# Kernel optimization log

Measured on AMD Instinct MI355X. Metric: run time of the kernel, lower is better.

Reference implementation:

```python
import jax, jax.numpy as jnp
import numpy as np

B_, N_, D_ = 8, 1024, 64
H_, DH_ = 4, 16
DI_, DS_, DTR_ = 128, 64, 4
MAXP = 512


def _ln(x, w, b, eps=1e-5):
    m = jnp.mean(x, -1, keepdims=True)
    v = jnp.mean((x - m) ** 2, -1, keepdims=True)
    return (x - m) * jax.lax.rsqrt(v + eps) * w + b


def _attn(x, drop_mask, Wq, Wkv, Wo, bo, rel_emb):
    b, n, d = x.shape
    scale = DH_ ** -0.5
    q = (x @ Wq).reshape(b, n, H_, DH_).transpose(0, 2, 1, 3)
    kv = x @ Wkv
    k = kv[..., :d].reshape(b, n, H_, DH_).transpose(0, 2, 1, 3)
    v = kv[..., d:].reshape(b, n, H_, DH_).transpose(0, 2, 1, 3)
    dots = jnp.einsum('bhid,bhjd->bhij', q, k) * scale
    seq = jnp.arange(n)
    dist = jnp.clip(seq[:, None] - seq[None, :], -MAXP, MAXP) + MAXP
    rpe = rel_emb[dist]  # (n, n, DH_)
    dots = dots + jnp.einsum('bhid,ijd->bhij', q, rpe) * scale
    # stochastic key drop: Bernoulli(0.3) positions get -1e12
    dots = dots + drop_mask.astype(dots.dtype) * (-1e12)
    attn = jax.nn.softmax(dots, axis=-1)
    out = jnp.einsum('bhij,bhjd->bhid', attn, v)
    out = out.transpose(0, 2, 1, 3).reshape(b, n, H_ * DH_)
    return out @ Wo + bo


def _mamba(x, W_in, conv_w, conv_b, W_xproj, W_dt, b_dt, A_log, Dm, W_out):
    b, n, _ = x.shape
    xz = x @ W_in                      # (b, n, 2*DI_)
    u, z = xz[..., :DI_], xz[..., DI_:]
    uc = u.transpose(0, 2, 1)          # (b, DI_, n)
    uc = jax.lax.conv_general_dilated(
        uc, conv_w[:, None, :], (1,), ((3, 0),),
        feature_group_count=DI_, dimension_numbers=('NCH', 'OIH', 'NCH'))
    uc = uc + conv_b[None, :, None]
    u = jax.nn.silu(uc).transpose(0, 2, 1)  # (b, n, DI_)
    xdb = u @ W_xproj                  # (b, n, DTR_+2*DS_)
    dt = jax.nn.softplus(xdb[..., :DTR_] @ W_dt + b_dt)  # (b, n, DI_)
    Bm = xdb[..., DTR_:DTR_ + DS_]
    Cm = xdb[..., DTR_ + DS_:]
    A = -jnp.exp(A_log)                # (DI_, DS_)

    def step(h, inp):
        dt_t, B_t, C_t, u_t = inp      # (b,DI_),(b,DS_),(b,DS_),(b,DI_)
        dA = jnp.exp(dt_t[..., None] * A)
        h = h * dA + (dt_t * u_t)[..., None] * B_t[:, None, :]
        y = jnp.einsum('bds,bs->bd', h, C_t)
        return h, y

    h0 = jnp.zeros((b, DI_, DS_), x.dtype)
    xs = (dt.transpose(1, 0, 2), Bm.transpose(1, 0, 2),
          Cm.transpose(1, 0, 2), u.transpose(1, 0, 2))
    _, ys = jax.lax.scan(step, h0, xs)
    y = ys.transpose(1, 0, 2) + u * Dm
    y = y * jax.nn.silu(z)
    return y @ W_out


def _rmsgn(x, gamma, eps=1e-5, groups=4):
    shp = x.shape
    dpg = shp[-1] // groups
    xg = x.reshape(shp[:-1] + (groups, dpg))
    rms = jnp.sqrt(jnp.sum(xg * xg, -1, keepdims=True)) * (dpg ** -0.5)
    return (xg / (rms + eps)).reshape(shp) * gamma


def _ff1(x, c1_w, c1_b, d1_w, d1_b):
    # SwiGLUConvDeconv1d(64, 256, kernel=4, shift=1); x: (b, s2, 64)
    s2 = x.shape[1]
    xc = x.transpose(0, 2, 1)
    xc = jnp.pad(xc, ((0, 0), (0, 0), (3, 3)))
    xc = jax.lax.conv_general_dilated(
        xc, c1_w, (1,), 'VALID', dimension_numbers=('NCH', 'OIH', 'NCH'))
    xc = xc + c1_b[None, :, None]
    gate = jax.nn.silu(xc[:, 256:, :])
    xc = xc[:, :256, :] * gate
    # ConvTranspose1d stride 1 == conv with flipped kernel, full padding
    w = jnp.flip(d1_w, -1).transpose(1, 0, 2)  # (64, 256, 4)
    xc = jax.lax.conv_general_dilated(
        xc, w, (1,), ((3, 3),), dimension_numbers=('NCH', 'OIH', 'NCH'))
    xc = xc + d1_b[None, :, None]
    out = xc.transpose(0, 2, 1)
    return out[:, 3:3 + s2, :]


def _forward(x, drop_mask, ln1_w, ln1_b, Wq, Wkv, Wo, bo, rel_emb,
             ln2_w, ln2_b, W_in, conv_w, conv_b, W_xproj, W_dt, b_dt,
             A_log, Dm, W_out, gamma, c1_w, c1_b, d1_w, d1_b, ln3_w, ln3_b):
    xt = _ln(x, ln1_w, ln1_b)
    xt = _attn(xt, drop_mask, Wq, Wkv, Wo, bo, rel_emb) + x
    x = x + xt  # dropout p=0 -> identity (faithful to original residual math)
    xt = _ln(x, ln2_w, ln2_b)
    m = _mamba(xt, W_in, conv_w, conv_b, W_xproj, W_dt, b_dt, A_log, Dm, W_out)
    m = jnp.where(m >= 0, m, 0.01 * m)  # leaky_relu
    m = _rmsgn(m, gamma)
    m = m + 0.5 * _ff1(m, c1_w, c1_b, d1_w, d1_b)
    x = x + m
    return _ln(x, ln3_w, ln3_b)


def setup_inputs() -> dict:
    ks = jax.random.split(jax.random.key(0), 16)
    g = lambda i, shp, s: jax.random.normal(ks[i], shp, dtype=jnp.float32) * s
    A_log = jnp.log(jnp.tile(jnp.arange(1, DS_ + 1, dtype=jnp.float32)[None, :], (DI_, 1)))
    return {
        'x': jax.random.normal(ks[0], (B_, N_, D_), dtype=jnp.float32),
        'drop_mask': jax.random.bernoulli(ks[1], 0.3, (B_, H_, N_, N_)),
        'ln1_w': jnp.ones((D_,), jnp.float32), 'ln1_b': jnp.zeros((D_,), jnp.float32),
        'Wq': g(2, (D_, D_), 0.1), 'Wkv': g(3, (D_, 2 * D_), 0.1),
        'Wo': g(4, (D_, D_), 0.1), 'bo': jnp.zeros((D_,), jnp.float32),
        'rel_emb': g(5, (2 * MAXP + 1, DH_), 0.02),
        'ln2_w': jnp.ones((D_,), jnp.float32), 'ln2_b': jnp.zeros((D_,), jnp.float32),
        'W_in': g(6, (D_, 2 * DI_), 0.1),
        'conv_w': g(7, (DI_, 4), 0.2), 'conv_b': jnp.zeros((DI_,), jnp.float32),
        'W_xproj': g(8, (DI_, DTR_ + 2 * DS_), 0.1),
        'W_dt': g(9, (DTR_, DI_), 0.1), 'b_dt': jnp.zeros((DI_,), jnp.float32),
        'A_log': A_log, 'Dm': jnp.ones((DI_,), jnp.float32),
        'W_out': g(10, (DI_, D_), 0.1),
        'gamma': jnp.ones((D_,), jnp.float32),
        'c1_w': g(11, (512, 64, 4), 0.1), 'c1_b': jnp.zeros((512,), jnp.float32),
        'd1_w': g(12, (256, 64, 4), 0.1), 'd1_b': jnp.zeros((64,), jnp.float32),
        'ln3_w': jnp.ones((D_,), jnp.float32), 'ln3_b': jnp.zeros((D_,), jnp.float32),
    }


def reference(x, drop_mask, ln1_w, ln1_b, Wq, Wkv, Wo, bo, rel_emb,
              ln2_w, ln2_b, W_in, conv_w, conv_b, W_xproj, W_dt, b_dt,
              A_log, Dm, W_out, gamma, c1_w, c1_b, d1_w, d1_b, ln3_w, ln3_b):
    return _forward(x, drop_mask, ln1_w, ln1_b, Wq, Wkv, Wo, bo, rel_emb,
                    ln2_w, ln2_b, W_in, conv_w, conv_b, W_xproj, W_dt, b_dt,
                    A_log, Dm, W_out, gamma, c1_w, c1_b, d1_w, d1_b, ln3_w, ln3_b)
```

## Files before the change

### kernel.cpp

```cpp
#include <hip/hip_runtime.h>
#include <math.h>


__device__ __forceinline__ float wsum64(float v){
#pragma unroll
  for(int m=32;m>0;m>>=1) v += __shfl_xor(v, m, 64);
  return v;
}
__device__ __forceinline__ float wmax64(float v){
#pragma unroll
  for(int m=32;m>0;m>>=1) v = fmaxf(v, __shfl_xor(v, m, 64));
  return v;
}
__device__ __forceinline__ float silu_f(float x){ return x / (1.f + __expf(-x)); }

__global__ __launch_bounds__(256) void k_ln1_qkv(
    const float* __restrict__ x, const float* __restrict__ w1, const float* __restrict__ b1,
    const float* __restrict__ Wq, const float* __restrict__ Wkv,
    const float* __restrict__ rel, const float* __restrict__ c1w,
    float* __restrict__ qb, float2* __restrict__ kvT,
    float* __restrict__ relT, float* __restrict__ c1wT){
  int lane = threadIdx.x & 63, warp = threadIdx.x >> 6;
  int token = blockIdx.x*4 + warp;
  __shared__ float xt[4][64];
  float xv = x[(size_t)token*64 + lane];
  float mean = wsum64(xv) * 0.015625f;
  float dlt = xv - mean;
  float var = wsum64(dlt*dlt) * 0.015625f;
  float xn = dlt * rsqrtf(var + 1e-5f) * w1[lane] + b1[lane];
  xt[warp][lane] = xn;
  __syncthreads();
  float aq=0.f, ak=0.f, av=0.f;
#pragma unroll 4
  for(int dd=0; dd<64; ++dd){
    float xd = xt[warp][dd];
    aq += xd * Wq[dd*64 + lane];
    ak += xd * Wkv[dd*128 + lane];
    av += xd * Wkv[dd*128 + 64 + lane];
  }
  int b = token >> 10, i = token & 1023;
  int h = lane >> 4, dh = lane & 15;
  size_t o  = (((size_t)(b*4 + h))*1024 + i)*16 + dh;
  size_t oT = (((size_t)(b*4 + h))*16 + dh)*1024 + i;
  qb[o]=aq;
  kvT[oT] = make_float2(ak, av);

  if (blockIdx.x < 65){
    int idx = blockIdx.x*256 + threadIdx.x;
    if (idx < 16*1025){
      int c = idx / 1025;
      int d = idx - c*1025;
      relT[idx] = rel[d*16 + c];
    }
  } else if (blockIdx.x < 577){
    int idx = (blockIdx.x-65)*256 + threadIdx.x;
    int row = idx >> 9;
    int ii  = idx & 511;
    c1wT[idx] = c1w[(size_t)ii*256 + row];
  }
}

__global__ __launch_bounds__(256) void k_kmax_pack(
    const float2* __restrict__ kvT, float* __restrict__ Kmax,
    const int* __restrict__ dmask, unsigned long long* __restrict__ mask64){
  int tid = threadIdx.x;
  if (blockIdx.x >= 32){
    size_t base = (size_t)(blockIdx.x - 32) * 16384;
    const int* dp = dmask + base;
    unsigned long long* mp = mask64 + (base >> 6);
#pragma unroll 4
    for(int r=0;r<64;++r){
      int m = dp[r*256 + tid];
      unsigned long long bal = __ballot(m != 0);
      if ((tid & 63) == 0) mp[r*4 + (tid >> 6)] = bal;
    }
    return;
  }
  int bh = blockIdx.x;
  const float2* base = kvT + (size_t)bh*16*1024;
  float mx = 0.f;
#pragma unroll
  for(int r=0;r<4;++r){
    int j = tid + 256*r;
    float ss = 0.f;
#pragma unroll
    for(int c=0;c<16;++c){ float2 kv = base[c*1024 + j]; ss += kv.x*kv.x; }
    mx = fmaxf(mx, ss);
  }
  mx = wmax64(mx);
  __shared__ float red[4];
  int lane = tid&63, wv = tid>>6;
  if(lane==0) red[wv]=mx;
  __syncthreads();
  if(tid==0) Kmax[bh] = sqrtf(fmaxf(fmaxf(red[0],red[1]),fmaxf(red[2],red[3])));
}

__global__ __launch_bounds__(256, 3) void k_attn(
    const float* __restrict__ qb, const float2* __restrict__ kvT,
    const unsigned long long* __restrict__ mask64, const float* __restrict__ relT,
    const float* __restrict__ Kmax, float* __restrict__ attn_raw){
  int tid = threadIdx.x;
  int lane = tid & 63, wv = tid >> 6;
  int wg   = blockIdx.x;
  int xcd  = wg & 7;
  int slot = wg >> 3;
  int bh   = xcd*4 + (slot >> 7);
  int i0   = (slot & 127) * 8;
  int b = bh >> 2, h = bh & 3;
  int r0 = wv*2, r1 = wv*2 + 1;

  __shared__ float Gc[8][1024];
  __shared__ float qs[8][16];
  __shared__ float G0s[8], G1024s[8];
  __shared__ float gmS[8];
  __shared__ float Ms[8];
  __shared__ float sums[8];

  if (tid < 128){
    int r = tid >> 4, c = tid & 15;
    qs[r][c] = qb[((size_t)bh*1024 + i0 + r)*16 + c] * 0.25f;
  }
  __syncthreads();

#pragma unroll 1
  for(int bb=0; bb<5; ++bb){
    int d = tid + 256*bb;
    if (d <= 1024){
      float rl[16];
#pragma unroll
      for(int c=0;c<16;++c) rl[c] = relT[c*1025 + d];
#pragma unroll
      for(int r=0;r<8;++r){
        float g = 0.f;
#pragma unroll
        for(int c=0;c<16;++c) g += qs[r][c]*rl[c];
        if (d == 0)        G0s[r] = g;
        else if (d == 1024) G1024s[r] = g;
        else {
          int j = i0 + r + 512 - d;
          if (j >= 0 && j < 1024) Gc[r][j] = g;
        }
      }
    }
  }
  __syncthreads();
  {
    const unsigned long long* mrow = mask64 + ((size_t)bh*1024 + i0)*16;
#pragma unroll
    for(int r=0;r<8;++r){
      float g0 = G0s[r], g1 = G1024s[r];
      int lo = i0 + r - 512;
      int hi = i0 + r + 512;
#pragma unroll
      for(int p=0;p<4;++p){
        int j = tid + 256*p;
        unsigned long long w = mrow[r*16 + (j>>6)];
        float g;
        if (j >= hi) g = g0;
        else if (j <= lo) g = g1;
        else g = Gc[r][j];
        if ((w >> (j & 63)) & 1ULL) g = -1e30f;
        Gc[r][j] = g;
      }
    }
  }
  __syncthreads();
  {
    int r = tid >> 5, jb = tid & 31;
    float gm = -3.0e38f;
#pragma unroll
    for(int k=0;k<32;++k) gm = fmaxf(gm, Gc[r][jb + 32*k]);
#pragma unroll
    for(int m=1;m<32;m<<=1) gm = fmaxf(gm, __shfl_xor(gm, m, 64));
    if ((lane&31)==0) gmS[r] = gm;
  }
  __syncthreads();
  if (tid < 8){
    float qn = 0.f;
#pragma unroll
    for(int c=0;c<16;++c) qn += qs[tid][c]*qs[tid][c];
    Ms[tid] = gmS[tid] + sqrtf(qn)*Kmax[bh];
  }
  __syncthreads();

  float q0[16], q1[16];
#pragma unroll
  for(int c=0;c<16;++c){ q0[c]=qs[r0][c]; q1[c]=qs[r1][c]; }
  float M0 = Ms[r0], M1 = Ms[r1];

  const float2* kvb = kvT + (size_t)bh*16*1024;

  float s0=0.f, s1=0.f;
  float a0[16], a1[16];
#pragma unroll
  for(int c=0;c<16;++c){ a0[c]=0.f; a1[c]=0.f; }

#pragma unroll 1
  for(int t=0;t<16;++t){
    int j = lane + 64*t;
    float2 kv[16];
#pragma unroll
    for(int c=0;c<16;++c) kv[c] = kvb[c*1024 + j];
    float sv0 = Gc[r0][j], sv1 = Gc[r1][j];
#pragma unroll
    for(int c=0;c<16;++c){ sv0 += q0[c]*kv[c].x; sv1 += q1[c]*kv[c].x; }
    float p0 = __expf(sv0 - M0);
    float p1 = __expf(sv1 - M1);
    s0 += p0; s1 += p1;
#pragma unroll
    for(int c=0;c<16;++c){ a0[c] += p0*kv[c].y; a1[c] += p1*kv[c].y; }
  }
  s0 = wsum64(s0); s1 = wsum64(s1);
#pragma unroll
  for(int c=0;c<16;++c){
    float x0 = a0[c];
    x0 += __shfl_xor(x0, 32, 64); x0 += __shfl_xor(x0, 16, 64);
    a0[c] = x0;
    float x1 = a1[c];
    x1 += __shfl_xor(x1, 32, 64); x1 += __shfl_xor(x1, 16, 64);
    a1[c] = x1;
  }
  __syncthreads();
  float* red = &Gc[0][0];
  if (lane < 16){
#pragma unroll
    for(int c=0;c<16;++c){
      red[r0*272 + lane*17 + c] = a0[c];
      red[r1*272 + lane*17 + c] = a1[c];
    }
  }
  if (lane == 0){ sums[r0] = s0; sums[r1] = s1; }
  __syncthreads();
  if (tid < 128){
    int row = tid >> 4, c = tid & 15;
    float tot = 0.f;
#pragma unroll
    for(int g=0; g<16; ++g) tot += red[row*272 + g*17 + c];
    attn_raw[((size_t)b*1024 + i0 + row)*64 + h*16 + c] = tot / sums[row];
  }
}

__global__ __launch_bounds__(256) void k_post_attn(
    const float* __restrict__ x, const float* __restrict__ attn_raw,
    const float* __restrict__ Wo, const float* __restrict__ bo,
    const float* __restrict__ ln2w, const float* __restrict__ ln2b,
    const float* __restrict__ W_in,
    float* __restrict__ x2, float* __restrict__ u0, float* __restrict__ zsarr){
  int tid = threadIdx.x;
  int lane = tid & 63, wv = tid >> 6;
  int tok0 = blockIdx.x * 16;
  __shared__ float arS[16][64];
  __shared__ float lnS[16][64];
  for(int l = tid; l < 1024; l += 256)
    arS[l >> 6][l & 63] = attn_raw[(size_t)tok0*64 + l];
  __syncthreads();
#pragma unroll 1
  for(int tt = 0; tt < 4; ++tt){
    int tl = wv*4 + tt;
    int token = tok0 + tl;
    float acc = bo[lane];
#pragma unroll 4
    for(int dd = 0; dd < 64; ++dd) acc += arS[tl][dd] * Wo[dd*64 + lane];
    float t = 2.f*x[(size_t)token*64 + lane] + acc;
    x2[(size_t)token*64 + lane] = t;
    float mean = wsum64(t)*0.015625f;
    float dlt = t - mean;
    float var = wsum64(dlt*dlt)*0.015625f;
    lnS[tl][lane] = dlt*rsqrtf(var+1e-5f)*ln2w[lane] + ln2b[lane];
  }
  __syncthreads();
  int oc = tid;
  float w[64];
#pragma unroll
  for(int dd = 0; dd < 64; ++dd) w[dd] = W_in[dd*256 + oc];
  const float4* lnS4 = (const float4*)&lnS[0][0];
#pragma unroll 1
  for(int tl = 0; tl < 16; ++tl){
    float acc = 0.f;
#pragma unroll
    for(int d4 = 0; d4 < 16; ++d4){
      float4 l4 = lnS4[tl*16 + d4];
      acc += l4.x*w[4*d4] + l4.y*w[4*d4+1] + l4.z*w[4*d4+2] + l4.w*w[4*d4+3];
    }
    int token = tok0 + tl;
    if (oc < 128) u0[(size_t)token*128 + oc] = acc;
    else          zsarr[(size_t)token*128 + (oc-128)] = silu_f(acc);
  }
}

__global__ __launch_bounds__(256) void k_conv_proj(
    const float* __restrict__ u0, const float* __restrict__ conv_w, const float* __restrict__ conv_b,
    const float* __restrict__ W_xproj, const float* __restrict__ W_dt, const float* __restrict__ b_dt,
    float* __restrict__ uarr, float* __restrict__ Bmp, float* __restrict__ Cmp, float* __restrict__ dtarr){
  int sub = threadIdx.x >> 7, c = threadIdx.x & 127;
  int token = blockIdx.x*2 + sub;
  int b = token >> 10, i = token & 1023;
  __shared__ float us[2][128];
  __shared__ float dtin[2][4];
  float acc = conv_b[c];
#pragma unroll
  for(int k2=0;k2<4;++k2){
    int t2 = i - 3 + k2;
    if (t2 >= 0) acc += u0[((size_t)b*1024 + t2)*128 + c]*conv_w[c*4+k2];
  }
  float uv = silu_f(acc);
  uarr[(size_t)token*128 + c] = uv;
  us[sub][c] = uv;
  __syncthreads();
  float accA = 0.f, accB = 0.f;
  int cB = 128 + (c & 3);
#pragma unroll 4
  for(int dd=0; dd<128; ++dd){
    float xd = us[sub][dd];
    accA += xd * W_xproj[dd*132 + c];
    accB += xd * W_xproj[dd*132 + cB];
  }
  if (c < 4){ dtin[sub][c] = accA; Cmp[(size_t)token*64 + 60 + c] = accB; }
  else if (c < 68) Bmp[(size_t)token*64 + (c-4)] = accA;
  else             Cmp[(size_t)token*64 + (c-68)] = accA;
  __syncthreads();
  float dv = b_dt[c];
#pragma unroll
  for(int r2=0;r2<4;++r2) dv += dtin[sub][r2]*W_dt[r2*128 + c];
  dv = fmaxf(dv, 0.f) + log1pf(expf(-fabsf(dv)));
  dtarr[(size_t)token*128 + c] = dv;
}

__global__ __launch_bounds__(256) void k_scan_a(
    const float* __restrict__ dtarr, const float* __restrict__ uarr,
    const float* __restrict__ Bmp, const float* __restrict__ A_log,
    float* __restrict__ Parr, float* __restrict__ Rarr){
  int lane = threadIdx.x & 63, warp = threadIdx.x >> 6;
  int w = blockIdx.x*4 + warp;
  int c = w & 7, d = (w >> 3) & 127, b = w >> 10;
  float A = -expf(A_log[d*64 + lane]);
  int tb = c*128;
  const float* dtp = dtarr + ((size_t)b*1024 + tb)*128 + d;
  const float* up  = uarr  + ((size_t)b*1024 + tb)*128 + d;
  const float* Bp  = Bmp   + ((size_t)b*1024 + tb)*64 + lane;
  float R = 0.f, sdt = 0.f;
  for(int t0=0; t0<128; t0+=8){
    float dtc[8], uc[8], Bc[8];
#pragma unroll
    for(int r=0;r<8;++r){
      dtc[r]=dtp[(size_t)(t0+r)*128]; uc[r]=up[(size_t)(t0+r)*128]; Bc[r]=Bp[(size_t)(t0+r)*64];
    }
#pragma unroll
    for(int r=0;r<8;++r){
      float dt = dtc[r];
      R = R*__expf(dt*A) + dt*uc[r]*Bc[r];
      sdt += dt;
    }
  }
  Parr[(size_t)w*64 + lane] = __expf(sdt*A);
  Rarr[(size_t)w*64 + lane] = R;
}

__global__ __launch_bounds__(256) void k_scan_c(
    const float* __restrict__ dtarr, const float* __restrict__ uarr,
    const float* __restrict__ Bmp, const float* __restrict__ Cmp,
    const float* __restrict__ zsarr, const float* __restrict__ A_log,
    const float* __restrict__ Dm, const float* __restrict__ Parr,
    const float* __restrict__ Rarr, float* __restrict__ ymp){
  int lane = threadIdx.x & 63, warp = threadIdx.x >> 6;
  int w = blockIdx.x*4 + warp;
  int c = w & 7, d = (w >> 3) & 127, b = w >> 10;
  float A = -expf(A_log[d*64 + lane]);
  float Dv = Dm[d];
  float h = 0.f;
  int wbase = w - c;
#pragma unroll 1
  for(int cp=0; cp<c; ++cp){
    float P = Parr[(size_t)(wbase+cp)*64 + lane];
    float R = Rarr[(size_t)(wbase+cp)*64 + lane];
    h = h*P + R;
  }
  int tb = c*128;
  const float* dtp = dtarr + ((size_t)b*1024 + tb)*128 + d;
  const float* up  = uarr  + ((size_t)b*1024 + tb)*128 + d;
  const float* zp  = zsarr + ((size_t)b*1024 + tb)*128 + d;
  const float* Bp  = Bmp   + ((size_t)b*1024 + tb)*64 + lane;
  const float* Cp  = Cmp   + ((size_t)b*1024 + tb)*64 + lane;
  float* yp        = ymp   + ((size_t)b*1024 + tb)*128 + d;
  for(int t0=0; t0<128; t0+=8){
    float dtc[8], uc[8], Bc[8], Cc[8], zc[8];
#pragma unroll
    for(int r=0;r<8;++r){
      dtc[r]=dtp[(size_t)(t0+r)*128]; uc[r]=up[(size_t)(t0+r)*128];
      Bc[r]=Bp[(size_t)(t0+r)*64];    Cc[r]=Cp[(size_t)(t0+r)*64];
      zc[r]=zp[(size_t)(t0+r)*128];
    }
    float hc[8];
#pragma unroll
    for(int r=0;r<8;++r){
      float dt = dtc[r];
      h = h*__expf(dt*A) + dt*uc[r]*Bc[r];
      hc[r] = h*Cc[r];
    }
    float y[8];
#pragma unroll
    for(int r=0;r<8;++r) y[r] = wsum64(hc[r]);
    if (lane==0){
#pragma unroll
      for(int r=0;r<8;++r) yp[(size_t)(t0+r)*128] = (y[r] + uc[r]*Dv)*zc[r];
    }
  }
}

__global__ __launch_bounds__(256) void k_wout(
    const float* __restrict__ ymp, const float* __restrict__ W_out,
    const float* __restrict__ gamma, float* __restrict__ marr){
  int lane = threadIdx.x & 63, warp = threadIdx.x >> 6;
  int token = blockIdx.x*4 + warp;
  __shared__ float ys[4][128];
  ys[warp][lane]      = ymp[(size_t)token*128 + lane];
  ys[warp][lane+64]   = ymp[(size_t)token*128 + 64 + lane];
  __syncthreads();
  float acc = 0.f;
#pragma unroll 4
  for(int dd=0; dd<128; ++dd) acc += ys[warp][dd]*W_out[dd*64 + lane];
  acc = acc >= 0.f ? acc : 0.01f*acc;
  float ss = acc*acc;
#pragma unroll
  for(int m=1;m<16;m<<=1) ss += __shfl_xor(ss, m, 64);
  float rms = sqrtf(ss)*0.25f;
  marr[(size_t)token*64 + lane] = acc/(rms + 1e-5f)*gamma[lane];
}

__global__ __launch_bounds__(256) void k_h2(
    const float* __restrict__ marr, const float* __restrict__ c1wT,
    const float* __restrict__ c1b, float* __restrict__ h2){
  int b = blockIdx.y;
  int t0 = blockIdx.x * 16;
  int tid = threadIdx.x;
  __shared__ float ms[19][64];
  for(int l = tid; l < 19*64; l += 256){
    int row = l >> 6, cc = l & 63;
    int t = t0 - 3 + row;
    ms[row][cc] = (t >= 0 && t < 1024) ? marr[((size_t)b*1024 + t)*64 + cc] : 0.f;
  }
  __syncthreads();
  int i = tid;
  float acc1[16], acc2[16];
#pragma unroll
  for(int tl=0;tl<16;++tl){ acc1[tl]=0.f; acc2[tl]=0.f; }
  for(int cc=0; cc<64; ++cc){
    float mv[19];
#pragma unroll
    for(int r2=0;r2<19;++r2) mv[r2] = ms[r2][cc];
    const float* wr = c1wT + (size_t)cc*4*512;
    float wa0 = wr[      i], wa1 = wr[ 512+i], wa2 = wr[1024+i], wa3 = wr[1536+i];
    float wg0 = wr[  256+i], wg1 = wr[ 768+i], wg2 = wr[1280+i], wg3 = wr[1792+i];
#pragma unroll
    for(int tl=0; tl<16; ++tl){
      acc1[tl] += wa0*mv[tl+0] + wa1*mv[tl+1] + wa2*mv[tl+2] + wa3*mv[tl+3];
      acc2[tl] += wg0*mv[tl+0] + wg1*mv[tl+1] + wg2*mv[tl+2] + wg3*mv[tl+3];
    }
  }
  float bb1 = c1b[i], bb2 = c1b[i+256];
#pragma unroll
  for(int tl=0; tl<16; ++tl){
    int t = t0 + tl;
    if (t < 1027){
      float o1 = acc1[tl] + bb1;
      float o2 = acc2[tl] + bb2;
      h2[((size_t)b*1027 + t)*256 + i] = o1 * silu_f(o2);
    }
  }
}

__global__ __launch_bounds__(256) void k_ff_final(
    const float* __restrict__ h2, const float* __restrict__ d1w, const float* __restrict__ d1b,
    const float* __restrict__ x2, const float* __restrict__ marr,
    const float* __restrict__ ln3w, const float* __restrict__ ln3b,
    float* __restrict__ out){
  int b = blockIdx.y;
  int s0 = blockIdx.x * 16;
  int tid = threadIdx.x;
  int o = tid & 63, sg = tid >> 6;
  __shared__ float hs[19][256];
  for(int l = tid; l < 19*256; l += 256){
    int row = l >> 8, cc = l & 255;
    hs[row][cc] = h2[((size_t)b*1027 + s0 + row)*256 + cc];
  }
  __syncthreads();
  int sl = sg*4;
  float acc0=0.f, acc1=0.f, acc2=0.f, acc3=0.f;
  const float4* wb = (const float4*)d1w + o;
#pragma unroll 2
  for(int i2=0; i2<256; ++i2){
    float4 wv = wb[(size_t)i2*64];
    float h0=hs[sl+0][i2], h1=hs[sl+1][i2], h2v=hs[sl+2][i2], h3=hs[sl+3][i2];
    float h4=hs[sl+4][i2], h5=hs[sl+5][i2], h6=hs[sl+6][i2];
    acc0 += h0*wv.w + h1*wv.z + h2v*wv.y + h3*wv.x;
    acc1 += h1*wv.w + h2v*wv.z + h3*wv.y + h4*wv.x;
    acc2 += h2v*wv.w + h3*wv.z + h4*wv.y + h5*wv.x;
    acc3 += h3*wv.w + h4*wv.z + h5*wv.y + h6*wv.x;
  }
  float accs[4] = {acc0, acc1, acc2, acc3};
  float bo_ = d1b[o];
#pragma unroll
  for(int r=0;r<4;++r){
    int s = s0 + sl + r;
    size_t idx = ((size_t)b*1024 + s)*64 + o;
    float tot = x2[idx] + marr[idx] + 0.5f*(accs[r] + bo_);
    float mean = wsum64(tot)*0.015625f;
    float dlt = tot - mean;
    float var = wsum64(dlt*dlt)*0.015625f;
    out[idx] = dlt*rsqrtf(var+1e-5f)*ln3w[o] + ln3b[o];
  }
}

extern "C" void kernel_launch(void* const* d_in, const int* in_sizes, int n_in,
                              void* d_out, int out_size, void* d_ws, size_t ws_size,
                              hipStream_t stream){
  const float* x       = (const float*)d_in[0];
  const int*   dmask   = (const int*)  d_in[1];
  const float* ln1w    = (const float*)d_in[2];
  const float* ln1b    = (const float*)d_in[3];
  const float* Wq      = (const float*)d_in[4];
  const float* Wkv     = (const float*)d_in[5];
  const float* Wo      = (const float*)d_in[6];
  const float* bo      = (const float*)d_in[7];
  const float* rel     = (const float*)d_in[8];
  const float* ln2w    = (const float*)d_in[9];
  const float* ln2b    = (const float*)d_in[10];
  const float* W_in    = (const float*)d_in[11];
  const float* conv_w  = (const float*)d_in[12];
  const float* conv_b  = (const float*)d_in[13];
  const float* W_xproj = (const float*)d_in[14];
  const float* W_dt    = (const float*)d_in[15];
  const float* b_dt    = (const float*)d_in[16];
  const float* A_log   = (const float*)d_in[17];
  const float* Dm      = (const float*)d_in[18];
  const float* W_out   = (const float*)d_in[19];
  const float* gamma   = (const float*)d_in[20];
  const float* c1w     = (const float*)d_in[21];
  const float* c1b     = (const float*)d_in[22];
  const float* d1w     = (const float*)d_in[23];
  const float* d1b     = (const float*)d_in[24];
  const float* ln3w    = (const float*)d_in[25];
  const float* ln3b    = (const float*)d_in[26];
  float* outp = (float*)d_out;

  float* ws = (float*)d_ws;
  float* qb       = ws;
  float* kvT      = qb      + 524288;
  float* attn_raw = kvT     + 1048576;
  float* x2       = attn_raw+ 524288;
  float* u0       = x2      + 524288;
  float* zsarr    = u0      + 1048576;
  float* uarr     = zsarr   + 1048576;
  float* dtarr    = uarr    + 1048576;
  float* Bmp      = dtarr   + 1048576;
  float* Cmp      = Bmp     + 524288;
  float* ymp      = Cmp     + 524288;
  float* marr     = ymp     + 1048576;
  float* h2       = marr    + 524288;
  float* relT     = h2      + 2103296;
  float* c1wT     = relT    + 16400;
  float* Parr     = c1wT    + 131072;
  float* Rarr     = Parr    + 524288;
  float* Kmaxa    = Rarr    + 524288;

  unsigned long long* mask64 = (unsigned long long*)h2;

  k_ln1_qkv  <<<2048, 256, 0, stream>>>(x, ln1w, ln1b, Wq, Wkv, rel, c1w,
                                        qb, (float2*)kvT, relT, c1wT);
  k_kmax_pack<<<2080, 256, 0, stream>>>((const float2*)kvT, Kmaxa, dmask, mask64);
  k_attn     <<<4096, 256, 0, stream>>>(qb, (const float2*)kvT, mask64, relT, Kmaxa, attn_raw);
  k_post_attn<<<512, 256, 0, stream>>>(x, attn_raw, Wo, bo, ln2w, ln2b, W_in, x2, u0, zsarr);
  k_conv_proj<<<4096, 256, 0, stream>>>(u0, conv_w, conv_b, W_xproj, W_dt, b_dt, uarr, Bmp, Cmp, dtarr);
  k_scan_a   <<<2048, 256, 0, stream>>>(dtarr, uarr, Bmp, A_log, Parr, Rarr);
  k_scan_c   <<<2048, 256, 0, stream>>>(dtarr, uarr, Bmp, Cmp, zsarr, A_log, Dm, Parr, Rarr, ymp);
  k_wout     <<<2048, 256, 0, stream>>>(ymp, W_out, gamma, marr);
  k_h2       <<<dim3(65,8), 256, 0, stream>>>(marr, c1wT, c1b, h2);
  k_ff_final <<<dim3(64,8), 256, 0, stream>>>(h2, d1w, d1b, x2, marr, ln3w, ln3b, outp);
}
```

Baseline: 769.0 us.

## Give each attention wave four query rows, prefetch K/V, move mask packing into QKV

The attention kernel drops to 128 threads per block, so each wavefront now handles four query rows instead of two. Each K/V load is reused across more rows, and the next K/V tile is double-buffered in registers. Mask bit-packing moves from the Kmax kernel into the LN1/QKV kernel as extra blocks, which leaves Kmax as a tiny 32-block launch. The risks are much higher register pressure (four 16-wide accumulators plus two K/V buffers) and lower occupancy. The Gc rows are also padded to 1032 floats.

Measured after the change: 748.8 us. 1.03x faster.

```diff
diff --git a/kernel.cpp b/kernel.cpp
--- a/kernel.cpp
+++ b/kernel.cpp
@@ -18,9 +18,24 @@
     const float* __restrict__ x, const float* __restrict__ w1, const float* __restrict__ b1,
     const float* __restrict__ Wq, const float* __restrict__ Wkv,
     const float* __restrict__ rel, const float* __restrict__ c1w,
+    const int* __restrict__ dmask,
     float* __restrict__ qb, float2* __restrict__ kvT,
-    float* __restrict__ relT, float* __restrict__ c1wT){
-  int lane = threadIdx.x & 63, warp = threadIdx.x >> 6;
+    float* __restrict__ relT, float* __restrict__ c1wT,
+    unsigned long long* __restrict__ mask64){
+  int tid = threadIdx.x;
+  if (blockIdx.x >= 2048){
+    size_t base = (size_t)(blockIdx.x - 2048) * 16384;
+    const int* dp = dmask + base;
+    unsigned long long* mp = mask64 + (base >> 6);
+#pragma unroll 4
+    for(int r=0;r<64;++r){
+      int m = dp[r*256 + tid];
+      unsigned long long bal = __ballot(m != 0);
+      if ((tid & 63) == 0) mp[r*4 + (tid >> 6)] = bal;
+    }
+    return;
+  }
+  int lane = tid & 63, warp = tid >> 6;
   int token = blockIdx.x*4 + warp;
   __shared__ float xt[4][64];
   float xv = x[(size_t)token*64 + lane];
@@ -46,36 +61,23 @@
   kvT[oT] = make_float2(ak, av);
 
   if (blockIdx.x < 65){
-    int idx = blockIdx.x*256 + threadIdx.x;
+    int idx = blockIdx.x*256 + tid;
     if (idx < 16*1025){
       int c = idx / 1025;
       int d = idx - c*1025;
       relT[idx] = rel[d*16 + c];
     }
   } else if (blockIdx.x < 577){
-    int idx = (blockIdx.x-65)*256 + threadIdx.x;
+    int idx = (blockIdx.x-65)*256 + tid;
     int row = idx >> 9;
     int ii  = idx & 511;
     c1wT[idx] = c1w[(size_t)ii*256 + row];
   }
 }
 
-__global__ __launch_bounds__(256) void k_kmax_pack(
-    const float2* __restrict__ kvT, float* __restrict__ Kmax,
-    const int* __restrict__ dmask, unsigned long long* __restrict__ mask64){
+__global__ __launch_bounds__(256) void k_kmax(
+    const float2* __restrict__ kvT, float* __restrict__ Kmax){
   int tid = threadIdx.x;
-  if (blockIdx.x >= 32){
-    size_t base = (size_t)(blockIdx.x - 32) * 16384;
-    const int* dp = dmask + base;
-    unsigned long long* mp = mask64 + (base >> 6);
-#pragma unroll 4
-    for(int r=0;r<64;++r){
-      int m = dp[r*256 + tid];
-      unsigned long long bal = __ballot(m != 0);
-      if ((tid & 63) == 0) mp[r*4 + (tid >> 6)] = bal;
-    }
-    return;
-  }
   int bh = blockIdx.x;
   const float2* base = kvT + (size_t)bh*16*1024;
   float mx = 0.f;
@@ -95,7 +97,7 @@
   if(tid==0) Kmax[bh] = sqrtf(fmaxf(fmaxf(red[0],red[1]),fmaxf(red[2],red[3])));
 }
 
-__global__ __launch_bounds__(256, 3) void k_attn(
+__global__ __launch_bounds__(128, 2) void k_attn(
     const float* __restrict__ qb, const float2* __restrict__ kvT,
     const unsigned long long* __restrict__ mask64, const float* __restrict__ relT,
     const float* __restrict__ Kmax, float* __restrict__ attn_raw){
@@ -107,24 +109,24 @@
   int bh   = xcd*4 + (slot >> 7);
   int i0   = (slot & 127) * 8;
   int b = bh >> 2, h = bh & 3;
-  int r0 = wv*2, r1 = wv*2 + 1;
-
-  __shared__ float Gc[8][1024];
+  int R0 = wv*4, R1 = R0+1, R2 = R0+2, R3 = R0+3;
+
+  __shared__ float Gc[8][1032];
   __shared__ float qs[8][16];
   __shared__ float G0s[8], G1024s[8];
   __shared__ float gmS[8];
   __shared__ float Ms[8];
   __shared__ float sums[8];
 
-  if (tid < 128){
+  {
     int r = tid >> 4, c = tid & 15;
     qs[r][c] = qb[((size_t)bh*1024 + i0 + r)*16 + c] * 0.25f;
   }
   __syncthreads();
 
 #pragma unroll 1
-  for(int bb=0; bb<5; ++bb){
-    int d = tid + 256*bb;
+  for(int bb=0; bb<9; ++bb){
+    int d = tid + 128*bb;
     if (d <= 1024){
       float rl[16];
 #pragma unroll
@@ -146,14 +148,14 @@
   __syncthreads();
   {
     const unsigned long long* mrow = mask64 + ((size_t)bh*1024 + i0)*16;
-#pragma unroll
+#pragma unroll 1
     for(int r=0;r<8;++r){
       float g0 = G0s[r], g1 = G1024s[r];
       int lo = i0 + r - 512;
       int hi = i0 + r + 512;
 #pragma unroll
-      for(int p=0;p<4;++p){
-        int j = tid + 256*p;
+      for(int p=0;p<8;++p){
+        int j = tid + 128*p;
         unsigned long long w = mrow[r*16 + (j>>6)];
         float g;
         if (j >= hi) g = g0;
@@ -166,13 +168,13 @@
   }
   __syncthreads();
   {
-    int r = tid >> 5, jb = tid & 31;
+    int r = tid >> 4, l4 = tid & 15;
     float gm = -3.0e38f;
 #pragma unroll
-    for(int k=0;k<32;++k) gm = fmaxf(gm, Gc[r][jb + 32*k]);
-#pragma unroll
-    for(int m=1;m<32;m<<=1) gm = fmaxf(gm, __shfl_xor(gm, m, 64));
-    if ((lane&31)==0) gmS[r] = gm;
+    for(int k=0;k<64;++k) gm = fmaxf(gm, Gc[r][l4 + 16*k]);
+#pragma unroll
+    for(int m=1;m<16;m<<=1) gm = fmaxf(gm, __shfl_xor(gm, m, 64));
+    if (l4 == 0) gmS[r] = gm;
   }
   __syncthreads();
   if (tid < 8){
@@ -183,55 +185,76 @@
   }
   __syncthreads();
 
-  float q0[16], q1[16];
-#pragma unroll
-  for(int c=0;c<16;++c){ q0[c]=qs[r0][c]; q1[c]=qs[r1][c]; }
-  float M0 = Ms[r0], M1 = Ms[r1];
+  float q0[16], q1[16], q2[16], q3[16];
+#pragma unroll
+  for(int c=0;c<16;++c){ q0[c]=qs[R0][c]; q1[c]=qs[R1][c]; q2[c]=qs[R2][c]; q3[c]=qs[R3][c]; }
+  float M0 = Ms[R0], M1 = Ms[R1], M2 = Ms[R2], M3 = Ms[R3];
 
   const float2* kvb = kvT + (size_t)bh*16*1024;
 
-  float s0=0.f, s1=0.f;
-  float a0[16], a1[16];
-#pragma unroll
-  for(int c=0;c<16;++c){ a0[c]=0.f; a1[c]=0.f; }
+  float s0=0.f, s1=0.f, s2=0.f, s3=0.f;
+  float a0[16], a1[16], a2[16], a3[16];
+#pragma unroll
+  for(int c=0;c<16;++c){ a0[c]=0.f; a1[c]=0.f; a2[c]=0.f; a3[c]=0.f; }
+
+  float2 kvA[16], kvB[16];
+  int j = lane;
+#pragma unroll
+  for(int c=0;c<16;++c) kvA[c] = kvb[c*1024 + j];
+
+#define ATTN_STEP(KV, JJ) do {                                              \
+    float sv0 = Gc[R0][JJ], sv1 = Gc[R1][JJ], sv2 = Gc[R2][JJ], sv3 = Gc[R3][JJ]; \
+    _Pragma("unroll")                                                       \
+    for(int c=0;c<16;++c){                                                  \
+      float kx = KV[c].x;                                                   \
+      sv0 += q0[c]*kx; sv1 += q1[c]*kx; sv2 += q2[c]*kx; sv3 += q3[c]*kx;   \
+    }                                                                       \
+    float p0 = __expf(sv0 - M0), p1 = __expf(sv1 - M1);                     \
+    float p2 = __expf(sv2 - M2), p3 = __expf(sv3 - M3);                     \
+    s0 += p0; s1 += p1; s2 += p2; s3 += p3;                                 \
+    _Pragma("unroll")                                                       \
+    for(int c=0;c<16;++c){                                                  \
+      float vy = KV[c].y;                                                   \
+      a0[c] += p0*vy; a1[c] += p1*vy; a2[c] += p2*vy; a3[c] += p3*vy;       \
+    }                                                                       \
+  } while(0)
 
 #pragma unroll 1
-  for(int t=0;t<16;++t){
-    int j = lane + 64*t;
-    float2 kv[16];
-#pragma unroll
-    for(int c=0;c<16;++c) kv[c] = kvb[c*1024 + j];
-    float sv0 = Gc[r0][j], sv1 = Gc[r1][j];
-#pragma unroll
-    for(int c=0;c<16;++c){ sv0 += q0[c]*kv[c].x; sv1 += q1[c]*kv[c].x; }
-    float p0 = __expf(sv0 - M0);
-    float p1 = __expf(sv1 - M1);
-    s0 += p0; s1 += p1;
-#pragma unroll
-    for(int c=0;c<16;++c){ a0[c] += p0*kv[c].y; a1[c] += p1*kv[c].y; }
-  }
-  s0 = wsum64(s0); s1 = wsum64(s1);
+  for(int t=0;t<16;t+=2){
+    int jb = (j + 64) & 1023;
+#pragma unroll
+    for(int c=0;c<16;++c) kvB[c] = kvb[c*1024 + jb];
+    ATTN_STEP(kvA, j);
+    int ja = (jb + 64) & 1023;
+#pragma unroll
+    for(int c=0;c<16;++c) kvA[c] = kvb[c*1024 + ja];
+    ATTN_STEP(kvB, jb);
+    j = ja;
+  }
+#undef ATTN_STEP
+
+  s0 = wsum64(s0); s1 = wsum64(s1); s2 = wsum64(s2); s3 = wsum64(s3);
 #pragma unroll
   for(int c=0;c<16;++c){
-    float x0 = a0[c];
-    x0 += __shfl_xor(x0, 32, 64); x0 += __shfl_xor(x0, 16, 64);
-    a0[c] = x0;
-    float x1 = a1[c];
-    x1 += __shfl_xor(x1, 32, 64); x1 += __shfl_xor(x1, 16, 64);
-    a1[c] = x1;
+    float x0 = a0[c]; x0 += __shfl_xor(x0,32,64); x0 += __shfl_xor(x0,16,64); a0[c] = x0;
+    float x1 = a1[c]; x1 += __shfl_xor(x1,32,64); x1 += __shfl_xor(x1,16,64); a1[c] = x1;
+    float x2 = a2[c]; x2 += __shfl_xor(x2,32,64); x2 += __shfl_xor(x2,16,64); a2[c] = x2;
+    float x3 = a3[c]; x3 += __shfl_xor(x3,32,64); x3 += __shfl_xor(x3,16,64); a3[c] = x3;
   }
   __syncthreads();
   float* red = &Gc[0][0];
   if (lane < 16){
 #pragma unroll
     for(int c=0;c<16;++c){
-      red[r0*272 + lane*17 + c] = a0[c];
-      red[r1*272 + lane*17 + c] = a1[c];
-    }
-  }
-  if (lane == 0){ sums[r0] = s0; sums[r1] = s1; }
-  __syncthreads();
-  if (tid < 128){
+      red[R0*272 + lane*17 + c] = a0[c];
+      red[R1*272 + lane*17 + c] = a1[c];
+      red[R2*272 + lane*17 + c] = a2[c];
+      red[R3*272 + lane*17 + c] = a3[c];
+    }
+  }
+  if (lane == 0){ sums[R0]=s0; sums[R1]=s1; sums[R2]=s2; sums[R3]=s3; }
+  __syncthreads();
+  {
     int row = tid >> 4, c = tid & 15;
     float tot = 0.f;
 #pragma unroll
@@ -565,10 +588,10 @@
 
   unsigned long long* mask64 = (unsigned long long*)h2;
 
-  k_ln1_qkv  <<<2048, 256, 0, stream>>>(x, ln1w, ln1b, Wq, Wkv, rel, c1w,
-                                        qb, (float2*)kvT, relT, c1wT);
-  k_kmax_pack<<<2080, 256, 0, stream>>>((const float2*)kvT, Kmaxa, dmask, mask64);
-  k_attn     <<<4096, 256, 0, stream>>>(qb, (const float2*)kvT, mask64, relT, Kmaxa, attn_raw);
+  k_ln1_qkv  <<<4096, 256, 0, stream>>>(x, ln1w, ln1b, Wq, Wkv, rel, c1w, dmask,
+                                        qb, (float2*)kvT, relT, c1wT, mask64);
+  k_kmax     <<<32, 256, 0, stream>>>((const float2*)kvT, Kmaxa);
+  k_attn     <<<4096, 128, 0, stream>>>(qb, (const float2*)kvT, mask64, relT, Kmaxa, attn_raw);
   k_post_attn<<<512, 256, 0, stream>>>(x, attn_raw, Wo, bo, ln2w, ln2b, W_in, x2, u0, zsarr);
   k_conv_proj<<<4096, 256, 0, stream>>>(u0, conv_w, conv_b, W_xproj, W_dt, b_dt, uarr, Bmp, Cmp, dtarr);
   k_scan_a   <<<2048, 256, 0, stream>>>(dtarr, uarr, Bmp, A_log, Parr, Rarr);
```
